# Kernel tuning notes

Hardware: AMD Instinct MI355X
Metric: run time of the kernel (lower is better)

Reference implementation:

```python
import jax, jax.numpy as jnp
import numpy as np

B, C, P, HP, WP = 128, 3, 196, 16, 16  # batch, channels, patches, patch h, patch w
E = 768  # embedding size; patches_pixel_count = C*HP*WP = 768


def setup_inputs() -> dict:
    key = jax.random.key(0)
    ks = jax.random.split(key, 9)
    return {
        "inputs": jax.random.normal(ks[0], (B, C, P, HP, WP), dtype=jnp.float32),
        "W1": jax.random.normal(ks[1], (C * HP * WP, 32), dtype=jnp.float32) * 0.02,
        "b1": jax.random.normal(ks[2], (32,), dtype=jnp.float32) * 0.02,
        "W2": jax.random.normal(ks[3], (32, 64), dtype=jnp.float32) * 0.02,
        "b2": jax.random.normal(ks[4], (64,), dtype=jnp.float32) * 0.02,
        "W3": jax.random.normal(ks[5], (64, E), dtype=jnp.float32) * 0.02,
        "b3": jax.random.normal(ks[6], (E,), dtype=jnp.float32) * 0.02,
        "cls_token": jax.random.normal(ks[7], (1, E), dtype=jnp.float32) * 0.02,
        "pos_enc": jax.random.normal(ks[8], (P + 1, E), dtype=jnp.float32) * 0.02,
    }


def reference(inputs, W1, b1, W2, b2, W3, b3, cls_token, pos_enc):
    b, c, p, hp, wp = inputs.shape
    # per-patch slab is [C, hp, wp] flattened in (C, h, w) order -> [B, P, C*hp*wp]
    x = jnp.transpose(inputs, (0, 2, 1, 3, 4)).reshape(b, p, c * hp * wp)
    x = x @ W1 + b1          # [B, P, 32]
    x = x @ W2 + b2          # [B, P, 64]
    x = x @ W3 + b3          # [B, P, E]
    cls = jnp.broadcast_to(cls_token[None], (b, 1, cls_token.shape[-1]))
    x = jnp.concatenate([cls, x], axis=1)  # [B, P+1, E]
    return x + pos_enc[None]               # broadcast add of position encodings
```

## Files before the change

### kernel.cpp

```cpp
#include <hip/hip_runtime.h>


#define BATCH 128
#define CH    3
#define NP    196
#define PIX   256
#define K1    768
#define N1    32
#define N2    64
#define EMB   768

typedef __bf16 bf16x8 __attribute__((ext_vector_type(8)));
typedef float  f32x4  __attribute__((ext_vector_type(4)));

#define W1T_OFF  0
#define W2T_OFF  49152
#define W3T_OFF  (49152 + 4096)
#define POSB_OFF (53248 + 98304)

__global__ void patchembed_prep(const float* __restrict__ W1, const float* __restrict__ W2,
                                const float* __restrict__ W3, const float* __restrict__ b3,
                                const float* __restrict__ cls, const float* __restrict__ pos,
                                __bf16* __restrict__ w1t, __bf16* __restrict__ w2t,
                                __bf16* __restrict__ w3t, float* __restrict__ posb,
                                float* __restrict__ out)
{
    int i = blockIdx.x * blockDim.x + threadIdx.x;
    const int T1 = K1 * N1;
    const int T2 = T1 + N1 * N2;
    const int T3 = T2 + N2 * EMB;
    const int T4 = T3 + 197 * EMB;
    const int T5 = T4 + BATCH * EMB;

    if (i < T1) {
        int n = i / K1, k = i - n * K1;
        w1t[i] = (__bf16)W1[k * N1 + n];
    } else if (i < T2) {
        int j = i - T1;
        int n = j / N1, k = j - n * N1;
        w2t[j] = (__bf16)W2[k * N2 + n];
    } else if (i < T3) {
        int j = i - T2;
        int n = j / N2, k = j - n * N2;
        w3t[j] = (__bf16)W3[k * EMB + n];
    } else if (i < T4) {
        int j = i - T3;
        int r = j / EMB, c = j - r * EMB;
        float base = (r == 0) ? cls[c] : b3[c];
        posb[j] = base + pos[j];
    } else if (i < T5) {
        int j = i - T4;
        int b = j / EMB, c = j - b * EMB;
        out[b * (197 * EMB) + c] = cls[c] + pos[c];
    }
}

__global__ __launch_bounds__(256) void patchembed_main(
    const float* __restrict__ X,
    const float* __restrict__ b1,
    const float* __restrict__ b2,
    const __bf16* __restrict__ w1t,
    const __bf16* __restrict__ w2t,
    const __bf16* __restrict__ w3t,
    const float* __restrict__ posb,
    float* __restrict__ out)
{
    __shared__ __align__(16) float  h1p[4][16][36];
    __shared__ __align__(16) __bf16 h2s[16][72];

    const int tid  = threadIdx.x;
    const int wv   = tid >> 6;
    const int lane = tid & 63;
    const int l15  = lane & 15;
    const int q    = lane >> 4;
    const int r0   = blockIdx.x * 16;

    {
        const int xrow  = r0 + l15;
        const int b     = xrow / NP;
        const int p     = xrow - b * NP;
        const int base0 = ((b * CH) * NP + p) * PIX;
        const __bf16* w0r = w1t + l15 * K1;
        const __bf16* w1r = w1t + (16 + l15) * K1;

        f32x4 acc0 = {0.f, 0.f, 0.f, 0.f};
        f32x4 acc1 = {0.f, 0.f, 0.f, 0.f};
        #pragma unroll
        for (int t = 0; t < 6; ++t) {
            const int kb  = wv * 6 + t;
            const int c   = kb >> 3;
            const int off = (kb & 7) * 32 + q * 8;
            const float4* xp = (const float4*)(X + base0 + c * (NP * PIX) + off);
            float4 u = xp[0];
            float4 v = xp[1];
            bf16x8 a;
            a[0] = (__bf16)u.x; a[1] = (__bf16)u.y; a[2] = (__bf16)u.z; a[3] = (__bf16)u.w;
            a[4] = (__bf16)v.x; a[5] = (__bf16)v.y; a[6] = (__bf16)v.z; a[7] = (__bf16)v.w;
            bf16x8 f0 = *(const bf16x8*)(w0r + kb * 32 + q * 8);
            bf16x8 f1 = *(const bf16x8*)(w1r + kb * 32 + q * 8);
            acc0 = __builtin_amdgcn_mfma_f32_16x16x32_bf16(a, f0, acc0, 0, 0, 0);
            acc1 = __builtin_amdgcn_mfma_f32_16x16x32_bf16(a, f1, acc1, 0, 0, 0);
        }
        #pragma unroll
        for (int r = 0; r < 4; ++r) {
            h1p[wv][q * 4 + r][l15]      = acc0[r];
            h1p[wv][q * 4 + r][16 + l15] = acc1[r];
        }
    }
    __syncthreads();

    {
        f32x4 s0 = {0.f, 0.f, 0.f, 0.f};
        f32x4 s1 = {0.f, 0.f, 0.f, 0.f};
        #pragma unroll
        for (int w = 0; w < 4; ++w) {
            s0 += *(const f32x4*)&h1p[w][l15][q * 8];
            s1 += *(const f32x4*)&h1p[w][l15][q * 8 + 4];
        }
        s0 += *(const f32x4*)(b1 + q * 8);
        s1 += *(const f32x4*)(b1 + q * 8 + 4);
        bf16x8 a;
        #pragma unroll
        for (int j = 0; j < 4; ++j) {
            a[j]     = (__bf16)s0[j];
            a[4 + j] = (__bf16)s1[j];
        }
        bf16x8 f = *(const bf16x8*)(w2t + (wv * 16 + l15) * N1 + q * 8);
        f32x4 z = {0.f, 0.f, 0.f, 0.f};
        f32x4 h2 = __builtin_amdgcn_mfma_f32_16x16x32_bf16(a, f, z, 0, 0, 0);
        const float bias = b2[wv * 16 + l15];
        #pragma unroll
        for (int r = 0; r < 4; ++r)
            h2s[q * 4 + r][wv * 16 + l15] = (__bf16)(h2[r] + bias);
    }
    __syncthreads();

    {
        bf16x8 a0 = *(const bf16x8*)(&h2s[l15][q * 8]);
        bf16x8 a1 = *(const bf16x8*)(&h2s[l15][32 + q * 8]);

        int obase[4], pbase[4];
        #pragma unroll
        for (int r = 0; r < 4; ++r) {
            const int row = r0 + q * 4 + r;
            const int b = row / NP;
            const int p = row - b * NP;
            obase[r] = (b * 197 + p + 1) * EMB;
            pbase[r] = (p + 1) * EMB;
        }

        #pragma unroll 4
        for (int t = 0; t < 12; ++t) {
            const int col = wv * 192 + t * 16 + l15;
            const __bf16* wr = w3t + col * N2;
            bf16x8 f0 = *(const bf16x8*)(wr + q * 8);
            bf16x8 f1 = *(const bf16x8*)(wr + 32 + q * 8);
            f32x4 z = {0.f, 0.f, 0.f, 0.f};
            f32x4 c0 = __builtin_amdgcn_mfma_f32_16x16x32_bf16(a0, f0, z, 0, 0, 0);
            c0       = __builtin_amdgcn_mfma_f32_16x16x32_bf16(a1, f1, c0, 0, 0, 0);
            #pragma unroll
            for (int r = 0; r < 4; ++r) {
                out[obase[0 * 4 + r] + col] = c0[r] + posb[pbase[r] + col];
            }
        }
    }
}

extern "C" void kernel_launch(void* const* d_in, const int* in_sizes, int n_in,
                              void* d_out, int out_size, void* d_ws, size_t ws_size,
                              hipStream_t stream)
{
    const float* X   = (const float*)d_in[0];
    const float* W1  = (const float*)d_in[1];
    const float* b1  = (const float*)d_in[2];
    const float* W2  = (const float*)d_in[3];
    const float* b2  = (const float*)d_in[4];
    const float* W3  = (const float*)d_in[5];
    const float* b3  = (const float*)d_in[6];
    const float* cls = (const float*)d_in[7];
    const float* pos = (const float*)d_in[8];
    float* out = (float*)d_out;

    char* ws = (char*)d_ws;
    __bf16* w1t = (__bf16*)(ws + W1T_OFF);
    __bf16* w2t = (__bf16*)(ws + W2T_OFF);
    __bf16* w3t = (__bf16*)(ws + W3T_OFF);
    float*  posb = (float*)(ws + POSB_OFF);

    patchembed_prep<<<1271, 256, 0, stream>>>(W1, W2, W3, b3, cls, pos,
                                              w1t, w2t, w3t, posb, out);
    patchembed_main<<<1568, 256, 0, stream>>>(X, b1, b2, w1t, w2t, w3t, posb, out);
}
```

Baseline: 184.6 us.

## Fold first two linear layers into one weight and software-pipeline final GEMM

Precomputes W1@W2 and the combined bias in a prep kernel, so the main kernel runs one 768x64 projection instead of two chained GEMMs, dropping a syncthreads and an LDS round trip. The b1/b2 contribution through W3 is folded into the posb table. The main kernel also issues all X loads up front and double-buffers the W3 fragments and posb loads across column groups. In exchange it adds an extra prep kernel launch, doubles the per-row W1 MFMA work, and raises register pressure; bf16 rounding of the folded weight changes numerics slightly.

```diff
diff --git a/kernel.cpp b/kernel.cpp
--- a/kernel.cpp
+++ b/kernel.cpp
@@ -6,67 +6,79 @@
 #define NP    196
 #define PIX   256
 #define K1    768
-#define N1    32
-#define N2    64
+#define NH    64
 #define EMB   768
 
 typedef __bf16 bf16x8 __attribute__((ext_vector_type(8)));
 typedef float  f32x4  __attribute__((ext_vector_type(4)));
 
-#define W1T_OFF  0
-#define W2T_OFF  49152
-#define W3T_OFF  (49152 + 4096)
-#define POSB_OFF (53248 + 98304)
-
-__global__ void patchembed_prep(const float* __restrict__ W1, const float* __restrict__ W2,
-                                const float* __restrict__ W3, const float* __restrict__ b3,
-                                const float* __restrict__ cls, const float* __restrict__ pos,
-                                __bf16* __restrict__ w1t, __bf16* __restrict__ w2t,
-                                __bf16* __restrict__ w3t, float* __restrict__ posb,
-                                float* __restrict__ out)
-{
-    int i = blockIdx.x * blockDim.x + threadIdx.x;
-    const int T1 = K1 * N1;
-    const int T2 = T1 + N1 * N2;
-    const int T3 = T2 + N2 * EMB;
-    const int T4 = T3 + 197 * EMB;
-    const int T5 = T4 + BATCH * EMB;
-
+#define W12T_OFF 0
+#define W3T_OFF  98304
+#define B12_OFF  196608
+#define POSB_OFF 196864
+
+__global__ __launch_bounds__(256) void patchembed_prep1(
+    const float* __restrict__ W1, const float* __restrict__ W2,
+    const float* __restrict__ b1, const float* __restrict__ b2,
+    __bf16* __restrict__ w12t, float* __restrict__ b12)
+{
+    const int i = blockIdx.x * 256 + threadIdx.x;
+    if (i < NH * K1) {
+        const int n = i / K1, k = i - n * K1;
+        float s = 0.f;
+        #pragma unroll
+        for (int j = 0; j < 32; ++j) s += W1[k * 32 + j] * W2[j * NH + n];
+        w12t[i] = (__bf16)s;
+    } else if (i < NH * K1 + NH) {
+        const int n = i - NH * K1;
+        float s = b2[n];
+        #pragma unroll
+        for (int j = 0; j < 32; ++j) s += b1[j] * W2[j * NH + n];
+        b12[n] = s;
+    }
+}
+
+__global__ __launch_bounds__(256) void patchembed_prep2(
+    const float* __restrict__ W3, const float* __restrict__ b3,
+    const float* __restrict__ cls, const float* __restrict__ pos,
+    const float* __restrict__ b12,
+    __bf16* __restrict__ w3t, float* __restrict__ posb, float* __restrict__ out)
+{
+    const int i = blockIdx.x * 256 + threadIdx.x;
+    const int T1 = EMB * NH;
+    const int T2 = T1 + 197 * EMB;
+    const int T3 = T2 + BATCH * EMB;
     if (i < T1) {
-        int n = i / K1, k = i - n * K1;
-        w1t[i] = (__bf16)W1[k * N1 + n];
+        const int col = i >> 6, kk = i & 63;
+        w3t[i] = (__bf16)W3[kk * EMB + col];
     } else if (i < T2) {
-        int j = i - T1;
-        int n = j / N1, k = j - n * N1;
-        w2t[j] = (__bf16)W2[k * N2 + n];
+        const int j = i - T1;
+        const int r = j / EMB, c = j - r * EMB;
+        float v = pos[j];
+        if (r == 0) {
+            v += cls[c];
+        } else {
+            float s = b3[c];
+            #pragma unroll
+            for (int n = 0; n < NH; ++n) s += b12[n] * W3[n * EMB + c];
+            v += s;
+        }
+        posb[j] = v;
     } else if (i < T3) {
-        int j = i - T2;
-        int n = j / N2, k = j - n * N2;
-        w3t[j] = (__bf16)W3[k * EMB + n];
-    } else if (i < T4) {
-        int j = i - T3;
-        int r = j / EMB, c = j - r * EMB;
-        float base = (r == 0) ? cls[c] : b3[c];
-        posb[j] = base + pos[j];
-    } else if (i < T5) {
-        int j = i - T4;
-        int b = j / EMB, c = j - b * EMB;
+        const int j = i - T2;
+        const int b = j / EMB, c = j - b * EMB;
         out[b * (197 * EMB) + c] = cls[c] + pos[c];
     }
 }
 
-__global__ __launch_bounds__(256) void patchembed_main(
+__global__ __launch_bounds__(256, 4) void patchembed_main(
     const float* __restrict__ X,
-    const float* __restrict__ b1,
-    const float* __restrict__ b2,
-    const __bf16* __restrict__ w1t,
-    const __bf16* __restrict__ w2t,
+    const __bf16* __restrict__ w12t,
     const __bf16* __restrict__ w3t,
-    const float* __restrict__ posb,
+    const float*  __restrict__ posb,
     float* __restrict__ out)
 {
-    __shared__ __align__(16) float  h1p[4][16][36];
-    __shared__ __align__(16) __bf16 h2s[16][72];
+    __shared__ __align__(16) float h1p[4][16][68];
 
     const int tid  = threadIdx.x;
     const int wv   = tid >> 6;
@@ -75,95 +87,122 @@
     const int q    = lane >> 4;
     const int r0   = blockIdx.x * 16;
 
+    int obase[4], pbase[4];
+    #pragma unroll
+    for (int r = 0; r < 4; ++r) {
+        const int row = r0 + q * 4 + r;
+        const int b = row / NP, p = row - b * NP;
+        obase[r] = (b * 197 + p + 1) * EMB;
+        pbase[r] = (p + 1) * EMB;
+    }
+
     {
-        const int xrow  = r0 + l15;
-        const int b     = xrow / NP;
-        const int p     = xrow - b * NP;
-        const int base0 = ((b * CH) * NP + p) * PIX;
-        const __bf16* w0r = w1t + l15 * K1;
-        const __bf16* w1r = w1t + (16 + l15) * K1;
+        const int xrow = r0 + l15;
+        const int b = xrow / NP, p = xrow - b * NP;
+        const float* xb = X + ((b * CH) * NP + p) * PIX;
+        const int kb0 = wv * 6;
+
+        float4 u[6], v[6];
+        #pragma unroll
+        for (int t = 0; t < 6; ++t) {
+            const int kb = kb0 + t;
+            const float* ptr = xb + (kb >> 3) * (NP * PIX) + (kb & 7) * 32 + q * 8;
+            u[t] = *(const float4*)ptr;
+            v[t] = *(const float4*)(ptr + 4);
+        }
 
         f32x4 acc0 = {0.f, 0.f, 0.f, 0.f};
-        f32x4 acc1 = {0.f, 0.f, 0.f, 0.f};
+        f32x4 acc1 = acc0, acc2 = acc0, acc3 = acc0;
         #pragma unroll
         for (int t = 0; t < 6; ++t) {
-            const int kb  = wv * 6 + t;
-            const int c   = kb >> 3;
-            const int off = (kb & 7) * 32 + q * 8;
-            const float4* xp = (const float4*)(X + base0 + c * (NP * PIX) + off);
-            float4 u = xp[0];
-            float4 v = xp[1];
+            const int kb = kb0 + t;
             bf16x8 a;
-            a[0] = (__bf16)u.x; a[1] = (__bf16)u.y; a[2] = (__bf16)u.z; a[3] = (__bf16)u.w;
-            a[4] = (__bf16)v.x; a[5] = (__bf16)v.y; a[6] = (__bf16)v.z; a[7] = (__bf16)v.w;
-            bf16x8 f0 = *(const bf16x8*)(w0r + kb * 32 + q * 8);
-            bf16x8 f1 = *(const bf16x8*)(w1r + kb * 32 + q * 8);
+            a[0] = (__bf16)u[t].x; a[1] = (__bf16)u[t].y;
+            a[2] = (__bf16)u[t].z; a[3] = (__bf16)u[t].w;
+            a[4] = (__bf16)v[t].x; a[5] = (__bf16)v[t].y;
+            a[6] = (__bf16)v[t].z; a[7] = (__bf16)v[t].w;
+            const __bf16* wb = w12t + kb * 32 + q * 8;
+            bf16x8 f0 = *(const bf16x8*)(wb + l15 * K1);
+            bf16x8 f1 = *(const bf16x8*)(wb + (16 + l15) * K1);
+            bf16x8 f2 = *(const bf16x8*)(wb + (32 + l15) * K1);
+            bf16x8 f3 = *(const bf16x8*)(wb + (48 + l15) * K1);
             acc0 = __builtin_amdgcn_mfma_f32_16x16x32_bf16(a, f0, acc0, 0, 0, 0);
             acc1 = __builtin_amdgcn_mfma_f32_16x16x32_bf16(a, f1, acc1, 0, 0, 0);
+            acc2 = __builtin_amdgcn_mfma_f32_16x16x32_bf16(a, f2, acc2, 0, 0, 0);
+            acc3 = __builtin_amdgcn_mfma_f32_16x16x32_bf16(a, f3, acc3, 0, 0, 0);
         }
         #pragma unroll
         for (int r = 0; r < 4; ++r) {
             h1p[wv][q * 4 + r][l15]      = acc0[r];
             h1p[wv][q * 4 + r][16 + l15] = acc1[r];
+            h1p[wv][q * 4 + r][32 + l15] = acc2[r];
+            h1p[wv][q * 4 + r][48 + l15] = acc3[r];
         }
     }
     __syncthreads();
 
+    const int c0l = wv * 192 + l15;
+    bf16x8 F0[2][3], F1[2][3];
+    float  pb[2][3][4];
+
+#define LOADG(buf, g)                                                         \
+    {                                                                         \
+        _Pragma("unroll")                                                     \
+        for (int t = 0; t < 3; ++t) {                                         \
+            const int col = c0l + ((g) * 3 + t) * 16;                         \
+            const __bf16* wr = w3t + col * NH;                                \
+            F0[buf][t] = *(const bf16x8*)(wr + q * 8);                        \
+            F1[buf][t] = *(const bf16x8*)(wr + 32 + q * 8);                   \
+            _Pragma("unroll")                                                 \
+            for (int r = 0; r < 4; ++r) pb[buf][t][r] = posb[pbase[r] + col]; \
+        }                                                                     \
+    }
+
+    bf16x8 a0, a1;
+
+#define COMPG(buf, g)                                                         \
+    {                                                                         \
+        _Pragma("unroll")                                                     \
+        for (int t = 0; t < 3; ++t) {                                         \
+            const int col = c0l + ((g) * 3 + t) * 16;                         \
+            f32x4 z = {0.f, 0.f, 0.f, 0.f};                                   \
+            f32x4 c = __builtin_amdgcn_mfma_f32_16x16x32_bf16(a0, F0[buf][t], z, 0, 0, 0); \
+            c = __builtin_amdgcn_mfma_f32_16x16x32_bf16(a1, F1[buf][t], c, 0, 0, 0);       \
+            _Pragma("unroll")                                                 \
+            for (int r = 0; r < 4; ++r) out[obase[r] + col] = c[r] + pb[buf][t][r];        \
+        }                                                                     \
+    }
+
+    LOADG(0, 0)
+
     {
-        f32x4 s0 = {0.f, 0.f, 0.f, 0.f};
-        f32x4 s1 = {0.f, 0.f, 0.f, 0.f};
+        f32x4 s0a = {0.f, 0.f, 0.f, 0.f};
+        f32x4 s0b = s0a, s1a = s0a, s1b = s0a;
         #pragma unroll
         for (int w = 0; w < 4; ++w) {
-            s0 += *(const f32x4*)&h1p[w][l15][q * 8];
-            s1 += *(const f32x4*)&h1p[w][l15][q * 8 + 4];
-        }
-        s0 += *(const f32x4*)(b1 + q * 8);
-        s1 += *(const f32x4*)(b1 + q * 8 + 4);
-        bf16x8 a;
+            const float* hp = &h1p[w][l15][0];
+            s0a += *(const f32x4*)(hp + q * 8);
+            s0b += *(const f32x4*)(hp + q * 8 + 4);
+            s1a += *(const f32x4*)(hp + 32 + q * 8);
+            s1b += *(const f32x4*)(hp + 32 + q * 8 + 4);
+        }
         #pragma unroll
         for (int j = 0; j < 4; ++j) {
-            a[j]     = (__bf16)s0[j];
-            a[4 + j] = (__bf16)s1[j];
-        }
-        bf16x8 f = *(const bf16x8*)(w2t + (wv * 16 + l15) * N1 + q * 8);
-        f32x4 z = {0.f, 0.f, 0.f, 0.f};
-        f32x4 h2 = __builtin_amdgcn_mfma_f32_16x16x32_bf16(a, f, z, 0, 0, 0);
-        const float bias = b2[wv * 16 + l15];
-        #pragma unroll
-        for (int r = 0; r < 4; ++r)
-            h2s[q * 4 + r][wv * 16 + l15] = (__bf16)(h2[r] + bias);
-    }
-    __syncthreads();
-
-    {
-        bf16x8 a0 = *(const bf16x8*)(&h2s[l15][q * 8]);
-        bf16x8 a1 = *(const bf16x8*)(&h2s[l15][32 + q * 8]);
-
-        int obase[4], pbase[4];
-        #pragma unroll
-        for (int r = 0; r < 4; ++r) {
-            const int row = r0 + q * 4 + r;
-            const int b = row / NP;
-            const int p = row - b * NP;
-            obase[r] = (b * 197 + p + 1) * EMB;
-            pbase[r] = (p + 1) * EMB;
-        }
-
-        #pragma unroll 4
-        for (int t = 0; t < 12; ++t) {
-            const int col = wv * 192 + t * 16 + l15;
-            const __bf16* wr = w3t + col * N2;
-            bf16x8 f0 = *(const bf16x8*)(wr + q * 8);
-            bf16x8 f1 = *(const bf16x8*)(wr + 32 + q * 8);
-            f32x4 z = {0.f, 0.f, 0.f, 0.f};
-            f32x4 c0 = __builtin_amdgcn_mfma_f32_16x16x32_bf16(a0, f0, z, 0, 0, 0);
-            c0       = __builtin_amdgcn_mfma_f32_16x16x32_bf16(a1, f1, c0, 0, 0, 0);
-            #pragma unroll
-            for (int r = 0; r < 4; ++r) {
-                out[obase[0 * 4 + r] + col] = c0[r] + posb[pbase[r] + col];
-            }
-        }
-    }
+            a0[j] = (__bf16)s0a[j]; a0[4 + j] = (__bf16)s0b[j];
+            a1[j] = (__bf16)s1a[j]; a1[4 + j] = (__bf16)s1b[j];
+        }
+    }
+
+    LOADG(1, 1)
+    COMPG(0, 0)
+    LOADG(0, 2)
+    COMPG(1, 1)
+    LOADG(1, 3)
+    COMPG(0, 2)
+    COMPG(1, 3)
+
+#undef LOADG
+#undef COMPG
 }
 
 extern "C" void kernel_launch(void* const* d_in, const int* in_sizes, int n_in,
@@ -182,12 +221,12 @@
     float* out = (float*)d_out;
 
     char* ws = (char*)d_ws;
-    __bf16* w1t = (__bf16*)(ws + W1T_OFF);
-    __bf16* w2t = (__bf16*)(ws + W2T_OFF);
-    __bf16* w3t = (__bf16*)(ws + W3T_OFF);
+    __bf16* w12t = (__bf16*)(ws + W12T_OFF);
+    __bf16* w3t  = (__bf16*)(ws + W3T_OFF);
+    float*  b12  = (float*)(ws + B12_OFF);
     float*  posb = (float*)(ws + POSB_OFF);
 
-    patchembed_prep<<<1271, 256, 0, stream>>>(W1, W2, W3, b3, cls, pos,
-                                              w1t, w2t, w3t, posb, out);
-    patchembed_main<<<1568, 256, 0, stream>>>(X, b1, b2, w1t, w2t, w3t, posb, out);
-}
+    patchembed_prep1<<<193, 256, 0, stream>>>(W1, W2, b1, b2, w12t, b12);
+    patchembed_prep2<<<1167, 256, 0, stream>>>(W3, b3, cls, pos, b12, w3t, posb, out);
+    patchembed_main<<<1568, 256, 0, stream>>>(X, w12t, w3t, posb, out);
+}
```

Result: slower. 199.0 us (+7.8%).
